# Kernel optimization log

Measured on AMD Instinct MI355X. Metric: run time of the kernel, lower is better.

The kernel has to match this reference:

```python
import jax, jax.numpy as jnp
import numpy as np

# weight_dict {0:1,1:1,2:1,3:1} with similarity_pyramid=True -> w_l = 1/2^l
WEIGHTS = [1.0, 0.5, 0.25, 0.125]
WINS = [9, 9, 7, 5]
NCC_FACTOR = 100.0
N_LOSSES = 2  # ['mse', 'ncc']


def _sliding_sum(x, win, axis):
    """Box (ones-kernel) sliding-window sum along one axis, 'same' output via
    zero padding of win//2 on each side -- separable equivalent of the dense
    ones-kernel conv in the original NCC_loss."""
    pad = win // 2
    pw = [(0, 0)] * x.ndim
    pw[axis] = (pad + 1, pad)  # extra leading zero so cumsum diff gives window sums
    c = jnp.cumsum(jnp.pad(x, pw), axis=axis)
    n = x.shape[axis]
    hi = jax.lax.slice_in_dim(c, win, win + n, axis=axis)
    lo = jax.lax.slice_in_dim(c, 0, n, axis=axis)
    return hi - lo


def _box_sum(x, win):
    # x: [B,1,H,W]; 2D box filter == separable 1D sliding sums
    return _sliding_sum(_sliding_sum(x, win, 2), win, 3)


def _ncc_loss(y_pred, y_true, win):
    Ii, Ji = y_true, y_pred
    ws = float(win * win)
    I_sum = _box_sum(Ii, win)
    J_sum = _box_sum(Ji, win)
    I2_sum = _box_sum(Ii * Ii, win)
    J2_sum = _box_sum(Ji * Ji, win)
    IJ_sum = _box_sum(Ii * Ji, win)
    u_I = I_sum / ws
    u_J = J_sum / ws
    cross = IJ_sum - u_J * I_sum - u_I * J_sum + u_I * u_J * ws
    I_var = I2_sum - 2.0 * u_I * I_sum + u_I * u_I * ws
    J_var = J2_sum - 2.0 * u_J * J_sum + u_J * u_J * ws
    cc = cross * cross / (I_var * J_var + 1e-8)
    return -jnp.sum(jnp.mean(cc, axis=0)) / NCC_FACTOR


def _l2_loss(inp, tgt):
    # sum over spatial dims, mean over batch & channel
    return jnp.mean(jnp.sum((inp - tgt) ** 2, axis=(2, 3)))


def _hier_loss(y_hats, y):
    total = jnp.zeros((), dtype=y.dtype)
    levels = []
    for l, yh in enumerate(y_hats):
        if yh.shape == y.shape:
            yt = y
        else:
            # F.interpolate bilinear align_corners=False == half-pixel linear resize
            yt = jax.image.resize(y, yh.shape, method='linear', antialias=False)
        w = WEIGHTS[l]
        ll = (w * _l2_loss(yh, yt) + w * _ncc_loss(yh, yt, WINS[l])) / N_LOSSES
        levels.append(ll)
        total = total + ll
    return total, levels


def setup_inputs() -> dict:
    key = jax.random.key(0)
    ks = jax.random.split(key, 5)
    return {
        'y_hat_0': jax.random.uniform(ks[0], (32, 1, 512, 512), dtype=jnp.float32),
        'y_hat_1': jax.random.uniform(ks[1], (32, 1, 256, 256), dtype=jnp.float32),
        'y_hat_2': jax.random.uniform(ks[2], (32, 1, 128, 128), dtype=jnp.float32),
        'y_hat_3': jax.random.uniform(ks[3], (32, 1, 64, 64), dtype=jnp.float32),
        'y': jax.random.uniform(ks[4], (32, 1, 512, 512), dtype=jnp.float32),
    }


def reference(y_hat_0, y_hat_1, y_hat_2, y_hat_3, y):
    total, levels = _hier_loss([y_hat_0, y_hat_1, y_hat_2, y_hat_3], y)
    return (total, *levels)
```

## Files before the change

kernel.cpp:

```cpp
#include <hip/hip_runtime.h>

#define NT 256
#define RCHUNK 32
#define NSLOT 32
#define RWMAX (NT + 8)

__device__ __forceinline__ float ccval(float sI, float sJ, float sII, float sJJ,
                                       float sIJ, float inv_ws) {
    float cross = fmaf(-(sI * sJ), inv_ws, sIJ);
    float iv    = fmaf(-(sI * sI), inv_ws, sII);
    float jv    = fmaf(-(sJ * sJ), inv_ws, sJJ);
    float den   = fmaf(iv, jv, 1e-8f);
    return (cross * cross) * __builtin_amdgcn_rcpf(den);
}

struct St { float J, i0, i1, i2, i3; };

template<int W, int H, int WIN, int S, int CW>
__device__ __forceinline__ void level_block(const float* __restrict__ yh,
                                            const float* __restrict__ y,
                                            int sub, float* __restrict__ ws_acc,
                                            int level,
                                            float (*bufI)[RWMAX], float (*bufJ)[RWMAX])
{
    constexpr int HW  = WIN / 2;
    constexpr int RW  = CW + 2 * HW;
    constexpr int T   = RCHUNK + 2 * HW;
    constexpr int G   = (T + WIN - 1) / WIN;
    constexpr int NIT = G * WIN;
    constexpr int OFF = (S - 2) / 2;
    constexpr int WRAP = RW - NT;
    constexpr float INV_WS = 1.0f / (float)(WIN * WIN);

    constexpr int STRIPS = W / CW;
    constexpr int CHUNKS = H / RCHUNK;

    int b     = sub / (STRIPS * CHUNKS);
    int rem   = sub - b * (STRIPS * CHUNKS);
    int chunk = rem / STRIPS;
    int strip = rem - chunk * STRIPS;
    int r0 = chunk * RCHUNK;
    int c0 = strip * CW;

    const float* Jb = yh + (size_t)b * (W * H);
    const float* Yb = y  + (size_t)b * (512 * 512);

    int t  = threadIdx.x;
    int jA = c0 - HW + t;
    int jB = jA + NT;

    auto fetch = [&](int rr, int j, St& s) {
        s.J = 0.f; s.i0 = 0.f; s.i1 = 0.f; s.i2 = 0.f; s.i3 = 0.f;
        int r = r0 - HW + rr;
        if (rr < NIT && r >= 0 && r < H && j >= 0 && j < W) {
            s.J = Jb[(size_t)r * W + j];
            if constexpr (S == 1) {
                s.i0 = Yb[(size_t)r * 512 + j];
            } else {
                int yr = S * r + OFF;
                const float* p = Yb + (size_t)yr * 512 + (S * j + OFF);
                s.i0 = p[0]; s.i1 = p[1]; s.i2 = p[512]; s.i3 = p[513];
            }
        }
    };
    auto ival = [&](const St& s) -> float {
        if constexpr (S == 1) return s.i0;
        else return 0.25f * ((s.i0 + s.i1) + (s.i2 + s.i3));
    };

    float rI[WIN], rJ[WIN], rII[WIN], rJJ[WIN], rIJ[WIN];
#pragma unroll
    for (int k = 0; k < WIN; ++k) { rI[k]=0.f; rJ[k]=0.f; rII[k]=0.f; rJJ[k]=0.f; rIJ[k]=0.f; }
    float vI=0.f, vJ=0.f, vII=0.f, vJJ=0.f, vIJ=0.f;
    float l2acc = 0.f, ccacc = 0.f;

    St sA, sB;
    fetch(0, jA, sA);
    sB.J = 0.f; sB.i0 = 0.f; sB.i1 = 0.f; sB.i2 = 0.f; sB.i3 = 0.f;
    if constexpr (WRAP > 0) { if (t < WRAP) fetch(0, jB, sB); }

    for (int g = 0; g < G; ++g) {
#pragma unroll
        for (int u = 0; u < WIN; ++u) {
            int rr = g * WIN + u;
            float* bI = bufI[rr & 1];
            float* bJ = bufJ[rr & 1];

            bI[t] = ival(sA);
            bJ[t] = sA.J;
            if constexpr (WRAP > 0) {
                if (t < WRAP) { bI[t + NT] = ival(sB); bJ[t + NT] = sB.J; }
            }
            fetch(rr + 1, jA, sA);
            if constexpr (WRAP > 0) { if (t < WRAP) fetch(rr + 1, jB, sB); }
            __syncthreads();
            if (t < CW) {
                float sIs=0.f, sJs=0.f, sIIs=0.f, sJJs=0.f, sIJs=0.f, Ic=0.f, Jc=0.f;
#pragma unroll
                for (int k = 0; k < WIN; ++k) {
                    float I = bI[t + k];
                    float J = bJ[t + k];
                    if (k == HW) { Ic = I; Jc = J; }
                    sIs += I; sJs += J;
                    sIIs = fmaf(I, I, sIIs);
                    sJJs = fmaf(J, J, sJJs);
                    sIJs = fmaf(I, J, sIJs);
                }
                if (rr >= HW && rr < HW + RCHUNK) {
                    float d = Jc - Ic;
                    l2acc = fmaf(d, d, l2acc);
                }
                rI[u]=sIs; rJ[u]=sJs; rII[u]=sIIs; rJJ[u]=sJJs; rIJ[u]=sIJs;
                vI+=sIs; vJ+=sJs; vII+=sIIs; vJJ+=sJJs; vIJ+=sIJs;
                if (rr >= 2 * HW && rr < T) {
                    ccacc += ccval(vI, vJ, vII, vJJ, vIJ, INV_WS);
                    const int uo = (u + 1) % WIN;
                    vI-=rI[uo]; vJ-=rJ[uo]; vII-=rII[uo]; vJJ-=rJJ[uo]; vIJ-=rIJ[uo];
                }
            }
        }
    }

#pragma unroll
    for (int off = 32; off > 0; off >>= 1) {
        l2acc += __shfl_down(l2acc, off);
        ccacc += __shfl_down(ccacc, off);
    }
    int lane = t & 63;
    if (lane == 0) {
        int slot = (blockIdx.x * 4 + (t >> 6)) & (NSLOT - 1);
        atomicAdd(&ws_acc[(level * 2 + 0) * NSLOT + slot], l2acc);
        atomicAdd(&ws_acc[(level * 2 + 1) * NSLOT + slot], ccacc);
    }
}

__global__ __launch_bounds__(NT)
void hier_loss_kernel(const float* __restrict__ yh0, const float* __restrict__ yh1,
                      const float* __restrict__ yh2, const float* __restrict__ yh3,
                      const float* __restrict__ y, float* ws_acc)
{
    __shared__ float bufI[2][RWMAX];
    __shared__ float bufJ[2][RWMAX];
    int bid = blockIdx.x;
    if (bid < 1024) {
        level_block<512, 512, 9, 1, 256>(yh0, y, bid, ws_acc, 0, bufI, bufJ);
    } else if (bid < 1280) {
        level_block<256, 256, 9, 2, 256>(yh1, y, bid - 1024, ws_acc, 1, bufI, bufJ);
    } else if (bid < 1408) {
        level_block<128, 128, 7, 4, 128>(yh2, y, bid - 1280, ws_acc, 2, bufI, bufJ);
    } else {
        level_block<64, 64, 5, 8, 64>(yh3, y, bid - 1408, ws_acc, 3, bufI, bufJ);
    }
}

__global__ void hier_finalize_kernel(const float* __restrict__ ws_acc, float* __restrict__ out)
{
    if (threadIdx.x == 0 && blockIdx.x == 0) {
        const float wts[4] = {1.0f, 0.5f, 0.25f, 0.125f};
        float total = 0.f;
#pragma unroll
        for (int lv = 0; lv < 4; ++lv) {
            float l2s = 0.f, ccs = 0.f;
            for (int s = 0; s < NSLOT; ++s) {
                l2s += ws_acc[(lv * 2 + 0) * NSLOT + s];
                ccs += ws_acc[(lv * 2 + 1) * NSLOT + s];
            }
            float l2  = l2s / 32.0f;
            float ncc = -ccs / (32.0f * 100.0f);
            float ll  = wts[lv] * (l2 + ncc) * 0.5f;
            out[1 + lv] = ll;
            total += ll;
        }
        out[0] = total;
    }
}

extern "C" void kernel_launch(void* const* d_in, const int* in_sizes, int n_in,
                              void* d_out, int out_size, void* d_ws, size_t ws_size,
                              hipStream_t stream)
{
    const float* yh0 = (const float*)d_in[0];
    const float* yh1 = (const float*)d_in[1];
    const float* yh2 = (const float*)d_in[2];
    const float* yh3 = (const float*)d_in[3];
    const float* y   = (const float*)d_in[4];
    float* ws_acc = (float*)d_ws;
    float* out = (float*)d_out;

    hipMemsetAsync(ws_acc, 0, 8 * NSLOT * sizeof(float), stream);
    hier_loss_kernel<<<1472, NT, 0, stream>>>(yh0, yh1, yh2, yh3, y, ws_acc);
    hier_finalize_kernel<<<1, 64, 0, stream>>>(ws_acc, out);
}
```

Before: 106.2 us.

## Stage full rows into LDS with direct global-to-LDS loads and multi-row phases

```diff
diff --git a/kernel.cpp b/kernel.cpp
--- a/kernel.cpp
+++ b/kernel.cpp
@@ -3,7 +3,21 @@
 #define NT 256
 #define RCHUNK 32
 #define NSLOT 32
-#define RWMAX (NT + 8)
+#define AC 4
+
+typedef float f2 __attribute__((ext_vector_type(2)));
+typedef float f4v __attribute__((ext_vector_type(4)));
+
+__device__ __forceinline__ void gll16(const float* g, float* l) {
+    __builtin_amdgcn_global_load_lds(
+        (const __attribute__((address_space(1))) void*)g,
+        (__attribute__((address_space(3))) void*)l, 16, 0, 0);
+}
+__device__ __forceinline__ void gll4(const float* g, float* l) {
+    __builtin_amdgcn_global_load_lds(
+        (const __attribute__((address_space(1))) void*)g,
+        (__attribute__((address_space(3))) void*)l, 4, 0, 0);
+}
 
 __device__ __forceinline__ float ccval(float sI, float sJ, float sII, float sJJ,
                                        float sIJ, float inv_ws) {
@@ -14,110 +28,194 @@
     return (cross * cross) * __builtin_amdgcn_rcpf(den);
 }
 
-struct St { float J, i0, i1, i2, i3; };
-
-template<int W, int H, int WIN, int S, int CW>
-__device__ __forceinline__ void level_block(const float* __restrict__ yh,
-                                            const float* __restrict__ y,
-                                            int sub, float* __restrict__ ws_acc,
-                                            int level,
-                                            float (*bufI)[RWMAX], float (*bufJ)[RWMAX])
-{
-    constexpr int HW  = WIN / 2;
-    constexpr int RW  = CW + 2 * HW;
-    constexpr int T   = RCHUNK + 2 * HW;
-    constexpr int G   = (T + WIN - 1) / WIN;
-    constexpr int NIT = G * WIN;
-    constexpr int OFF = (S - 2) / 2;
-    constexpr int WRAP = RW - NT;
+template<int W, int WIN, int S, int P>
+__device__ __forceinline__ void stage_phase(
+    float* __restrict__ smem, int parity, int k, int t,
+    const float* __restrict__ Jb, const float* __restrict__ Yb, int r0)
+{
+    constexpr int HW = WIN / 2;
+    constexpr int T = RCHUNK + 2 * HW;
+    constexpr int ROWSZ = W + 16;
+    constexpr bool B16 = (W >= 256);
+    constexpr int SEGW = B16 ? 256 : 64;
+    constexpr int SEGS = W / SEGW;
+    constexpr int NARR = (S == 1) ? 2 : 1;
+    int wv = t >> 6, ln = t & 63;
+    int fl = 0;
+#pragma unroll
+    for (int p = 0; p < P; ++p) {
+        int rr = k * P + p;
+        int r = r0 - HW + rr;
+        bool valid = (rr < T) && (r >= 0) && (r < W);
+        float* base = smem + (size_t)((parity * P + p) * 2) * ROWSZ;
+#pragma unroll
+        for (int a = 0; a < NARR; ++a) {
+            const float* srow;
+            float* drow;
+            if (a == NARR - 1) { srow = Jb + (long)r * W;   drow = base + ROWSZ; }
+            else               { srow = Yb + (long)r * 512; drow = base; }
+#pragma unroll
+            for (int sg = 0; sg < SEGS; ++sg) {
+                if ((fl & 3) == wv) {
+                    if (valid) {
+                        if constexpr (B16) gll16(srow + sg * 256 + 4 * ln, drow + AC + sg * 256);
+                        else               gll4 (srow + sg * 64 + ln,      drow + AC + sg * 64);
+                    } else {
+                        if constexpr (B16) {
+                            f4v z = {0.f, 0.f, 0.f, 0.f};
+                            *(f4v*)(drow + AC + sg * 256 + 4 * ln) = z;
+                        } else {
+                            drow[AC + sg * 64 + ln] = 0.f;
+                        }
+                    }
+                }
+                ++fl;
+            }
+        }
+        if constexpr (S >= 2) {
+            if (t < W) {
+                float v = 0.f;
+                if (valid) {
+                    if constexpr (S == 2) {
+                        const float* pp = Yb + (long)(2 * r) * 512 + 2 * t;
+                        f2 a2 = *(const f2*)pp;
+                        f2 b2 = *(const f2*)(pp + 512);
+                        v = 0.25f * ((a2.x + a2.y) + (b2.x + b2.y));
+                    } else {
+                        constexpr int OFF = (S - 2) / 2;
+                        const float* pp = Yb + (long)(S * r + OFF) * 512 + (S * t + OFF);
+                        v = 0.25f * ((pp[0] + pp[1]) + (pp[512] + pp[513]));
+                    }
+                }
+                base[AC + t] = v;
+            }
+        }
+    }
+}
+
+template<int W, int WIN, int P, int BASE, int CPT>
+__device__ __forceinline__ void compute_rows(
+    const float* __restrict__ smem, int parity, int k, int t,
+    float (&rI)[CPT][WIN], float (&rJ)[CPT][WIN], float (&rII)[CPT][WIN],
+    float (&rJJ)[CPT][WIN], float (&rIJ)[CPT][WIN],
+    float (&vI)[CPT], float (&vJ)[CPT], float (&vII)[CPT],
+    float (&vJJ)[CPT], float (&vIJ)[CPT],
+    float& l2acc, float& ccacc)
+{
+    constexpr int HW = WIN / 2;
+    constexpr int T = RCHUNK + 2 * HW;
+    constexpr int ROWSZ = W + 16;
+    constexpr int NB = (WIN + 2) / 2;
     constexpr float INV_WS = 1.0f / (float)(WIN * WIN);
-
-    constexpr int STRIPS = W / CW;
-    constexpr int CHUNKS = H / RCHUNK;
-
-    int b     = sub / (STRIPS * CHUNKS);
-    int rem   = sub - b * (STRIPS * CHUNKS);
-    int chunk = rem / STRIPS;
-    int strip = rem - chunk * STRIPS;
+#pragma unroll
+    for (int u = 0; u < P; ++u) {
+        int rr = k * P + u;
+        const float* bI = smem + (size_t)((parity * P + u) * 2) * ROWSZ;
+        const float* bJ = bI + ROWSZ;
+        if (rr < T) {
+#pragma unroll
+            for (int c = 0; c < CPT; ++c) {
+                int col = t + c * NT;
+                if (CPT * NT <= W || col < W) {
+                    int START = col - HW + AC;
+                    int e0 = START & ~1;
+                    bool sh = (START & 1) != 0;
+                    float LI[2 * NB], LJ[2 * NB];
+#pragma unroll
+                    for (int kk = 0; kk < NB; ++kk) {
+                        f2 a2 = *(const f2*)(bI + e0 + 2 * kk);
+                        f2 b2 = *(const f2*)(bJ + e0 + 2 * kk);
+                        LI[2 * kk] = a2.x; LI[2 * kk + 1] = a2.y;
+                        LJ[2 * kk] = b2.x; LJ[2 * kk + 1] = b2.y;
+                    }
+                    float sIs = 0.f, sJs = 0.f, sIIs = 0.f, sJJs = 0.f, sIJs = 0.f;
+#pragma unroll
+                    for (int kk = 0; kk < WIN; ++kk) {
+                        float I = sh ? LI[kk + 1] : LI[kk];
+                        float J = sh ? LJ[kk + 1] : LJ[kk];
+                        sIs += I; sJs += J;
+                        sIIs = fmaf(I, I, sIIs);
+                        sJJs = fmaf(J, J, sJJs);
+                        sIJs = fmaf(I, J, sIJs);
+                    }
+                    if (rr >= HW && rr < HW + RCHUNK) {
+                        float Ic = sh ? LI[HW + 1] : LI[HW];
+                        float Jc = sh ? LJ[HW + 1] : LJ[HW];
+                        float d = Jc - Ic;
+                        l2acc = fmaf(d, d, l2acc);
+                    }
+                    const int SL = (BASE + u) % WIN;
+                    rI[c][SL] = sIs; rJ[c][SL] = sJs; rII[c][SL] = sIIs;
+                    rJJ[c][SL] = sJJs; rIJ[c][SL] = sIJs;
+                    vI[c] += sIs; vJ[c] += sJs; vII[c] += sIIs;
+                    vJJ[c] += sJJs; vIJ[c] += sIJs;
+                    if (rr >= 2 * HW) {
+                        ccacc += ccval(vI[c], vJ[c], vII[c], vJJ[c], vIJ[c], INV_WS);
+                        const int SO = (BASE + u + 1) % WIN;
+                        vI[c] -= rI[c][SO]; vJ[c] -= rJ[c][SO]; vII[c] -= rII[c][SO];
+                        vJJ[c] -= rJJ[c][SO]; vIJ[c] -= rIJ[c][SO];
+                    }
+                }
+            }
+        }
+    }
+}
+
+template<int W, int WIN, int S, int P, int CPT>
+__device__ void level_block(const float* __restrict__ yh, const float* __restrict__ y,
+                            int sub, float* __restrict__ ws_acc, int level, float* smem)
+{
+    constexpr int HW = WIN / 2;
+    constexpr int T = RCHUNK + 2 * HW;
+    constexpr int NPH = (T + P - 1) / P;
+    constexpr int RES = WIN / P;
+    constexpr int NMACRO = (NPH + RES - 1) / RES;
+    constexpr int ROWSZ = W + 16;
+    constexpr int SMN = 2 * P * 2 * ROWSZ;
+
+    int b = sub & 31;
+    int chunk = sub >> 5;
     int r0 = chunk * RCHUNK;
-    int c0 = strip * CW;
-
-    const float* Jb = yh + (size_t)b * (W * H);
-    const float* Yb = y  + (size_t)b * (512 * 512);
-
-    int t  = threadIdx.x;
-    int jA = c0 - HW + t;
-    int jB = jA + NT;
-
-    auto fetch = [&](int rr, int j, St& s) {
-        s.J = 0.f; s.i0 = 0.f; s.i1 = 0.f; s.i2 = 0.f; s.i3 = 0.f;
-        int r = r0 - HW + rr;
-        if (rr < NIT && r >= 0 && r < H && j >= 0 && j < W) {
-            s.J = Jb[(size_t)r * W + j];
-            if constexpr (S == 1) {
-                s.i0 = Yb[(size_t)r * 512 + j];
-            } else {
-                int yr = S * r + OFF;
-                const float* p = Yb + (size_t)yr * 512 + (S * j + OFF);
-                s.i0 = p[0]; s.i1 = p[1]; s.i2 = p[512]; s.i3 = p[513];
-            }
-        }
-    };
-    auto ival = [&](const St& s) -> float {
-        if constexpr (S == 1) return s.i0;
-        else return 0.25f * ((s.i0 + s.i1) + (s.i2 + s.i3));
-    };
-
-    float rI[WIN], rJ[WIN], rII[WIN], rJJ[WIN], rIJ[WIN];
-#pragma unroll
-    for (int k = 0; k < WIN; ++k) { rI[k]=0.f; rJ[k]=0.f; rII[k]=0.f; rJJ[k]=0.f; rIJ[k]=0.f; }
-    float vI=0.f, vJ=0.f, vII=0.f, vJJ=0.f, vIJ=0.f;
+    const float* Jb = yh + (size_t)b * W * W;
+    const float* Yb = y + (size_t)b * 512 * 512;
+    int t = threadIdx.x;
+
+    for (int i = t; i < SMN; i += NT) smem[i] = 0.f;
+    __syncthreads();
+
+    float rI[CPT][WIN], rJ[CPT][WIN], rII[CPT][WIN], rJJ[CPT][WIN], rIJ[CPT][WIN];
+    float vI[CPT], vJ[CPT], vII[CPT], vJJ[CPT], vIJ[CPT];
+#pragma unroll
+    for (int c = 0; c < CPT; ++c) {
+#pragma unroll
+        for (int kk = 0; kk < WIN; ++kk) {
+            rI[c][kk] = 0.f; rJ[c][kk] = 0.f; rII[c][kk] = 0.f;
+            rJJ[c][kk] = 0.f; rIJ[c][kk] = 0.f;
+        }
+        vI[c] = 0.f; vJ[c] = 0.f; vII[c] = 0.f; vJJ[c] = 0.f; vIJ[c] = 0.f;
+    }
     float l2acc = 0.f, ccacc = 0.f;
 
-    St sA, sB;
-    fetch(0, jA, sA);
-    sB.J = 0.f; sB.i0 = 0.f; sB.i1 = 0.f; sB.i2 = 0.f; sB.i3 = 0.f;
-    if constexpr (WRAP > 0) { if (t < WRAP) fetch(0, jB, sB); }
-
-    for (int g = 0; g < G; ++g) {
-#pragma unroll
-        for (int u = 0; u < WIN; ++u) {
-            int rr = g * WIN + u;
-            float* bI = bufI[rr & 1];
-            float* bJ = bufJ[rr & 1];
-
-            bI[t] = ival(sA);
-            bJ[t] = sA.J;
-            if constexpr (WRAP > 0) {
-                if (t < WRAP) { bI[t + NT] = ival(sB); bJ[t + NT] = sB.J; }
-            }
-            fetch(rr + 1, jA, sA);
-            if constexpr (WRAP > 0) { if (t < WRAP) fetch(rr + 1, jB, sB); }
-            __syncthreads();
-            if (t < CW) {
-                float sIs=0.f, sJs=0.f, sIIs=0.f, sJJs=0.f, sIJs=0.f, Ic=0.f, Jc=0.f;
-#pragma unroll
-                for (int k = 0; k < WIN; ++k) {
-                    float I = bI[t + k];
-                    float J = bJ[t + k];
-                    if (k == HW) { Ic = I; Jc = J; }
-                    sIs += I; sJs += J;
-                    sIIs = fmaf(I, I, sIIs);
-                    sJJs = fmaf(J, J, sJJs);
-                    sIJs = fmaf(I, J, sIJs);
-                }
-                if (rr >= HW && rr < HW + RCHUNK) {
-                    float d = Jc - Ic;
-                    l2acc = fmaf(d, d, l2acc);
-                }
-                rI[u]=sIs; rJ[u]=sJs; rII[u]=sIIs; rJJ[u]=sJJs; rIJ[u]=sIJs;
-                vI+=sIs; vJ+=sJs; vII+=sIIs; vJJ+=sJJs; vIJ+=sIJs;
-                if (rr >= 2 * HW && rr < T) {
-                    ccacc += ccval(vI, vJ, vII, vJJ, vIJ, INV_WS);
-                    const int uo = (u + 1) % WIN;
-                    vI-=rI[uo]; vJ-=rJ[uo]; vII-=rII[uo]; vJJ-=rJJ[uo]; vIJ-=rIJ[uo];
-                }
-            }
+    stage_phase<W, WIN, S, P>(smem, 0, 0, t, Jb, Yb, r0);
+
+    for (int m = 0; m < NMACRO; ++m) {
+#pragma unroll
+        for (int j = 0; j < RES; ++j) {
+            int k = m * RES + j;
+            asm volatile("s_waitcnt vmcnt(0) lgkmcnt(0)" ::: "memory");
+            __builtin_amdgcn_s_barrier();
+            asm volatile("" ::: "memory");
+            if (k + 1 < NPH)
+                stage_phase<W, WIN, S, P>(smem, (k + 1) & 1, k + 1, t, Jb, Yb, r0);
+            if (j == 0)
+                compute_rows<W, WIN, P, 0, CPT>(smem, k & 1, k, t, rI, rJ, rII, rJJ, rIJ,
+                                                vI, vJ, vII, vJJ, vIJ, l2acc, ccacc);
+            else if (j == 1)
+                compute_rows<W, WIN, P, (P) % WIN, CPT>(smem, k & 1, k, t, rI, rJ, rII, rJJ, rIJ,
+                                                        vI, vJ, vII, vJJ, vIJ, l2acc, ccacc);
+            else
+                compute_rows<W, WIN, P, (2 * P) % WIN, CPT>(smem, k & 1, k, t, rI, rJ, rII, rJJ, rIJ,
+                                                            vI, vJ, vII, vJJ, vIJ, l2acc, ccacc);
         }
     }
 
@@ -126,8 +224,7 @@
         l2acc += __shfl_down(l2acc, off);
         ccacc += __shfl_down(ccacc, off);
     }
-    int lane = t & 63;
-    if (lane == 0) {
+    if ((t & 63) == 0) {
         int slot = (blockIdx.x * 4 + (t >> 6)) & (NSLOT - 1);
         atomicAdd(&ws_acc[(level * 2 + 0) * NSLOT + slot], l2acc);
         atomicAdd(&ws_acc[(level * 2 + 1) * NSLOT + slot], ccacc);
@@ -139,17 +236,16 @@
                       const float* __restrict__ yh2, const float* __restrict__ yh3,
                       const float* __restrict__ y, float* ws_acc)
 {
-    __shared__ float bufI[2][RWMAX];
-    __shared__ float bufJ[2][RWMAX];
+    __shared__ float smem[6336];
     int bid = blockIdx.x;
-    if (bid < 1024) {
-        level_block<512, 512, 9, 1, 256>(yh0, y, bid, ws_acc, 0, bufI, bufJ);
-    } else if (bid < 1280) {
-        level_block<256, 256, 9, 2, 256>(yh1, y, bid - 1024, ws_acc, 1, bufI, bufJ);
-    } else if (bid < 1408) {
-        level_block<128, 128, 7, 4, 128>(yh2, y, bid - 1280, ws_acc, 2, bufI, bufJ);
+    if (bid < 512) {
+        level_block<512, 9, 1, 3, 2>(yh0, y, bid, ws_acc, 0, smem);
+    } else if (bid < 768) {
+        level_block<256, 9, 2, 3, 1>(yh1, y, bid - 512, ws_acc, 1, smem);
+    } else if (bid < 896) {
+        level_block<128, 7, 4, 7, 1>(yh2, y, bid - 768, ws_acc, 2, smem);
     } else {
-        level_block<64, 64, 5, 8, 64>(yh3, y, bid - 1408, ws_acc, 3, bufI, bufJ);
+        level_block<64, 5, 8, 5, 1>(yh3, y, bid - 896, ws_acc, 3, smem);
     }
 }
 
@@ -188,6 +284,6 @@
     float* out = (float*)d_out;
 
     hipMemsetAsync(ws_acc, 0, 8 * NSLOT * sizeof(float), stream);
-    hier_loss_kernel<<<1472, NT, 0, stream>>>(yh0, yh1, yh2, yh3, y, ws_acc);
+    hier_loss_kernel<<<960, NT, 0, stream>>>(yh0, yh1, yh2, yh3, y, ws_acc);
     hier_finalize_kernel<<<1, 64, 0, stream>>>(ws_acc, out);
 }
```

Result: slower. 283.7 us (+167.1%).

## Make each wavefront own a 64-column strip and drop block barriers

Applied to the files above, without the earlier changes.

```diff
diff --git a/kernel.cpp b/kernel.cpp
--- a/kernel.cpp
+++ b/kernel.cpp
@@ -3,7 +3,9 @@
 #define NT 256
 #define RCHUNK 32
 #define NSLOT 32
-#define RWMAX (NT + 8)
+#define RWA 72
+
+typedef float f2 __attribute__((ext_vector_type(2)));
 
 __device__ __forceinline__ float ccval(float sI, float sJ, float sII, float sJJ,
                                        float sIJ, float inv_ws) {
@@ -16,49 +18,47 @@
 
 struct St { float J, i0, i1, i2, i3; };
 
-template<int W, int H, int WIN, int S, int CW>
-__device__ __forceinline__ void level_block(const float* __restrict__ yh,
-                                            const float* __restrict__ y,
-                                            int sub, float* __restrict__ ws_acc,
-                                            int level,
-                                            float (*bufI)[RWMAX], float (*bufJ)[RWMAX])
-{
-    constexpr int HW  = WIN / 2;
-    constexpr int RW  = CW + 2 * HW;
-    constexpr int T   = RCHUNK + 2 * HW;
-    constexpr int G   = (T + WIN - 1) / WIN;
+template<int W, int WIN, int S>
+__device__ void level_wave(const float* __restrict__ yh,
+                           const float* __restrict__ y,
+                           int sub, float* __restrict__ ws_acc, int level,
+                           float* __restrict__ slab, int wid)
+{
+    constexpr int HW = WIN / 2;
+    constexpr int RW = 64 + 2 * HW;
+    constexpr int T  = RCHUNK + 2 * HW;
+    constexpr int G  = (T + WIN - 1) / WIN;
     constexpr int NIT = G * WIN;
+    constexpr int WRAP = RW - 64;
+    constexpr int NB = (WIN + 2) / 2;
     constexpr int OFF = (S - 2) / 2;
-    constexpr int WRAP = RW - NT;
     constexpr float INV_WS = 1.0f / (float)(WIN * WIN);
-
-    constexpr int STRIPS = W / CW;
-    constexpr int CHUNKS = H / RCHUNK;
+    constexpr int STRIPS = W / 64;
+    constexpr int CHUNKS = W / RCHUNK;
 
     int b     = sub / (STRIPS * CHUNKS);
     int rem   = sub - b * (STRIPS * CHUNKS);
     int chunk = rem / STRIPS;
     int strip = rem - chunk * STRIPS;
     int r0 = chunk * RCHUNK;
-    int c0 = strip * CW;
-
-    const float* Jb = yh + (size_t)b * (W * H);
-    const float* Yb = y  + (size_t)b * (512 * 512);
-
-    int t  = threadIdx.x;
-    int jA = c0 - HW + t;
-    int jB = jA + NT;
-
-    auto fetch = [&](int rr, int j, St& s) {
+    int c0 = strip * 64;
+
+    const float* Jb = yh + (size_t)b * W * W;
+    const float* Yb = y  + (size_t)b * 512 * 512;
+
+    int l  = threadIdx.x & 63;
+    int jA = c0 - HW + l;
+    int jB = jA + 64;
+
+    auto fetch1 = [&](int rr, int j, St& s) {
         s.J = 0.f; s.i0 = 0.f; s.i1 = 0.f; s.i2 = 0.f; s.i3 = 0.f;
         int r = r0 - HW + rr;
-        if (rr < NIT && r >= 0 && r < H && j >= 0 && j < W) {
-            s.J = Jb[(size_t)r * W + j];
+        if (rr < NIT && r >= 0 && r < W && j >= 0 && j < W) {
+            s.J = Jb[(long)r * W + j];
             if constexpr (S == 1) {
-                s.i0 = Yb[(size_t)r * 512 + j];
+                s.i0 = Yb[(long)r * 512 + j];
             } else {
-                int yr = S * r + OFF;
-                const float* p = Yb + (size_t)yr * 512 + (S * j + OFF);
+                const float* p = Yb + (long)(S * r + OFF) * 512 + (S * j + OFF);
                 s.i0 = p[0]; s.i1 = p[1]; s.i2 = p[512]; s.i3 = p[513];
             }
         }
@@ -75,44 +75,53 @@
     float l2acc = 0.f, ccacc = 0.f;
 
     St sA, sB;
-    fetch(0, jA, sA);
+    fetch1(0, jA, sA);
     sB.J = 0.f; sB.i0 = 0.f; sB.i1 = 0.f; sB.i2 = 0.f; sB.i3 = 0.f;
-    if constexpr (WRAP > 0) { if (t < WRAP) fetch(0, jB, sB); }
+    if (l < WRAP) fetch1(0, jB, sB);
 
     for (int g = 0; g < G; ++g) {
 #pragma unroll
         for (int u = 0; u < WIN; ++u) {
             int rr = g * WIN + u;
-            float* bI = bufI[rr & 1];
-            float* bJ = bufJ[rr & 1];
-
-            bI[t] = ival(sA);
-            bJ[t] = sA.J;
-            if constexpr (WRAP > 0) {
-                if (t < WRAP) { bI[t + NT] = ival(sB); bJ[t + NT] = sB.J; }
-            }
-            fetch(rr + 1, jA, sA);
-            if constexpr (WRAP > 0) { if (t < WRAP) fetch(rr + 1, jB, sB); }
-            __syncthreads();
-            if (t < CW) {
-                float sIs=0.f, sJs=0.f, sIIs=0.f, sJJs=0.f, sIJs=0.f, Ic=0.f, Jc=0.f;
-#pragma unroll
-                for (int k = 0; k < WIN; ++k) {
-                    float I = bI[t + k];
-                    float J = bJ[t + k];
-                    if (k == HW) { Ic = I; Jc = J; }
+            float* bI = slab + (size_t)(((rr & 1) * 2 + 0) * RWA);
+            float* bJ = slab + (size_t)(((rr & 1) * 2 + 1) * RWA);
+
+            bI[l] = ival(sA);
+            bJ[l] = sA.J;
+            if (l < WRAP) { bI[64 + l] = ival(sB); bJ[64 + l] = sB.J; }
+            fetch1(rr + 1, jA, sA);
+            if (l < WRAP) fetch1(rr + 1, jB, sB);
+            asm volatile("s_waitcnt lgkmcnt(0)" ::: "memory");
+            if (rr < T) {
+                int e0 = l & ~1;
+                bool sh = (l & 1) != 0;
+                float LI[2 * NB], LJ[2 * NB];
+#pragma unroll
+                for (int kk = 0; kk < NB; ++kk) {
+                    f2 a2 = *(const f2*)(bI + e0 + 2 * kk);
+                    f2 b2 = *(const f2*)(bJ + e0 + 2 * kk);
+                    LI[2 * kk] = a2.x; LI[2 * kk + 1] = a2.y;
+                    LJ[2 * kk] = b2.x; LJ[2 * kk + 1] = b2.y;
+                }
+                float sIs=0.f, sJs=0.f, sIIs=0.f, sJJs=0.f, sIJs=0.f;
+#pragma unroll
+                for (int kk = 0; kk < WIN; ++kk) {
+                    float I = sh ? LI[kk + 1] : LI[kk];
+                    float J = sh ? LJ[kk + 1] : LJ[kk];
                     sIs += I; sJs += J;
                     sIIs = fmaf(I, I, sIIs);
                     sJJs = fmaf(J, J, sJJs);
                     sIJs = fmaf(I, J, sIJs);
                 }
                 if (rr >= HW && rr < HW + RCHUNK) {
+                    float Ic = sh ? LI[HW + 1] : LI[HW];
+                    float Jc = sh ? LJ[HW + 1] : LJ[HW];
                     float d = Jc - Ic;
                     l2acc = fmaf(d, d, l2acc);
                 }
                 rI[u]=sIs; rJ[u]=sJs; rII[u]=sIIs; rJJ[u]=sJJs; rIJ[u]=sIJs;
                 vI+=sIs; vJ+=sJs; vII+=sIIs; vJJ+=sJJs; vIJ+=sIJs;
-                if (rr >= 2 * HW && rr < T) {
+                if (rr >= 2 * HW) {
                     ccacc += ccval(vI, vJ, vII, vJJ, vIJ, INV_WS);
                     const int uo = (u + 1) % WIN;
                     vI-=rI[uo]; vJ-=rJ[uo]; vII-=rII[uo]; vJJ-=rJJ[uo]; vIJ-=rIJ[uo];
@@ -126,9 +135,8 @@
         l2acc += __shfl_down(l2acc, off);
         ccacc += __shfl_down(ccacc, off);
     }
-    int lane = t & 63;
-    if (lane == 0) {
-        int slot = (blockIdx.x * 4 + (t >> 6)) & (NSLOT - 1);
+    if (l == 0) {
+        int slot = wid & (NSLOT - 1);
         atomicAdd(&ws_acc[(level * 2 + 0) * NSLOT + slot], l2acc);
         atomicAdd(&ws_acc[(level * 2 + 1) * NSLOT + slot], ccacc);
     }
@@ -139,17 +147,19 @@
                       const float* __restrict__ yh2, const float* __restrict__ yh3,
                       const float* __restrict__ y, float* ws_acc)
 {
-    __shared__ float bufI[2][RWMAX];
-    __shared__ float bufJ[2][RWMAX];
-    int bid = blockIdx.x;
-    if (bid < 1024) {
-        level_block<512, 512, 9, 1, 256>(yh0, y, bid, ws_acc, 0, bufI, bufJ);
-    } else if (bid < 1280) {
-        level_block<256, 256, 9, 2, 256>(yh1, y, bid - 1024, ws_acc, 1, bufI, bufJ);
-    } else if (bid < 1408) {
-        level_block<128, 128, 7, 4, 128>(yh2, y, bid - 1280, ws_acc, 2, bufI, bufJ);
+    __shared__ float smem[4][2][2][RWA];
+    int wave = threadIdx.x >> 6;
+    float* slab = &smem[wave][0][0][0];
+
+    int wid = blockIdx.x * (NT / 64) + wave;
+    if (wid < 4096) {
+        level_wave<512, 9, 1>(yh0, y, wid, ws_acc, 0, slab, wid);
+    } else if (wid < 5120) {
+        level_wave<256, 9, 2>(yh1, y, wid - 4096, ws_acc, 1, slab, wid);
+    } else if (wid < 5376) {
+        level_wave<128, 7, 4>(yh2, y, wid - 5120, ws_acc, 2, slab, wid);
     } else {
-        level_block<64, 64, 5, 8, 64>(yh3, y, bid - 1408, ws_acc, 3, bufI, bufJ);
+        level_wave<64, 5, 8>(yh3, y, wid - 5376, ws_acc, 3, slab, wid);
     }
 }
 
@@ -188,6 +198,6 @@
     float* out = (float*)d_out;
 
     hipMemsetAsync(ws_acc, 0, 8 * NSLOT * sizeof(float), stream);
-    hier_loss_kernel<<<1472, NT, 0, stream>>>(yh0, yh1, yh2, yh3, y, ws_acc);
+    hier_loss_kernel<<<5440 / (NT / 64), NT, 0, stream>>>(yh0, yh1, yh2, yh3, y, ws_acc);
     hier_finalize_kernel<<<1, 64, 0, stream>>>(ws_acc, out);
 }
```

Result: slower. 215.7 us (+103.1%).

## Batch row fetches into WIN-row phases with double-buffered interleaved LDS

Applied to the files above, without the earlier changes.

```diff
diff --git a/kernel.cpp b/kernel.cpp
--- a/kernel.cpp
+++ b/kernel.cpp
@@ -3,7 +3,9 @@
 #define NT 256
 #define RCHUNK 32
 #define NSLOT 32
-#define RWMAX (NT + 8)
+#define RWA 272
+
+typedef float f2 __attribute__((ext_vector_type(2)));
 
 __device__ __forceinline__ float ccval(float sI, float sJ, float sII, float sJJ,
                                        float sIJ, float inv_ws) {
@@ -14,26 +16,21 @@
     return (cross * cross) * __builtin_amdgcn_rcpf(den);
 }
 
-struct St { float J, i0, i1, i2, i3; };
-
-template<int W, int H, int WIN, int S, int CW>
-__device__ __forceinline__ void level_block(const float* __restrict__ yh,
-                                            const float* __restrict__ y,
-                                            int sub, float* __restrict__ ws_acc,
-                                            int level,
-                                            float (*bufI)[RWMAX], float (*bufJ)[RWMAX])
+template<int W, int WIN, int S, int CW>
+__device__ void level_block(const float* __restrict__ yh,
+                            const float* __restrict__ y,
+                            int sub, float* __restrict__ ws_acc, int level,
+                            float* __restrict__ sm)
 {
     constexpr int HW  = WIN / 2;
     constexpr int RW  = CW + 2 * HW;
     constexpr int T   = RCHUNK + 2 * HW;
-    constexpr int G   = (T + WIN - 1) / WIN;
-    constexpr int NIT = G * WIN;
+    constexpr int NPH = (T + WIN - 1) / WIN;
     constexpr int OFF = (S - 2) / 2;
-    constexpr int WRAP = RW - NT;
+    constexpr int WRAP = (RW > NT) ? (RW - NT) : 0;
     constexpr float INV_WS = 1.0f / (float)(WIN * WIN);
-
     constexpr int STRIPS = W / CW;
-    constexpr int CHUNKS = H / RCHUNK;
+    constexpr int CHUNKS = W / RCHUNK;
 
     int b     = sub / (STRIPS * CHUNKS);
     int rem   = sub - b * (STRIPS * CHUNKS);
@@ -42,30 +39,53 @@
     int r0 = chunk * RCHUNK;
     int c0 = strip * CW;
 
-    const float* Jb = yh + (size_t)b * (W * H);
-    const float* Yb = y  + (size_t)b * (512 * 512);
-
-    int t  = threadIdx.x;
-    int jA = c0 - HW + t;
-    int jB = jA + NT;
-
-    auto fetch = [&](int rr, int j, St& s) {
-        s.J = 0.f; s.i0 = 0.f; s.i1 = 0.f; s.i2 = 0.f; s.i3 = 0.f;
+    const float* Jb = yh + (size_t)b * W * W;
+    const float* Yb = y  + (size_t)b * 512 * 512;
+    int t = threadIdx.x;
+    int colA = c0 - HW + t;
+    int colB = colA + NT;
+
+    float fI[WIN], fJ[WIN], gI[WIN], gJ[WIN];
+
+    auto fetch_one = [&](int rr, int col, float& I, float& J) {
+        I = 0.f; J = 0.f;
         int r = r0 - HW + rr;
-        if (rr < NIT && r >= 0 && r < H && j >= 0 && j < W) {
-            s.J = Jb[(size_t)r * W + j];
+        if (rr < T && r >= 0 && r < W && col >= 0 && col < W) {
+            J = Jb[(long)r * W + col];
             if constexpr (S == 1) {
-                s.i0 = Yb[(size_t)r * 512 + j];
+                I = Yb[(long)r * 512 + col];
+            } else if constexpr (S == 2) {
+                const float* p = Yb + (long)(2 * r) * 512 + 2 * col;
+                f2 a = *(const f2*)p;
+                f2 c = *(const f2*)(p + 512);
+                I = 0.25f * ((a.x + a.y) + (c.x + c.y));
             } else {
-                int yr = S * r + OFF;
-                const float* p = Yb + (size_t)yr * 512 + (S * j + OFF);
-                s.i0 = p[0]; s.i1 = p[1]; s.i2 = p[512]; s.i3 = p[513];
+                const float* p = Yb + (long)(S * r + OFF) * 512 + (S * col + OFF);
+                I = 0.25f * ((p[0] + p[1]) + (p[512] + p[513]));
             }
         }
     };
-    auto ival = [&](const St& s) -> float {
-        if constexpr (S == 1) return s.i0;
-        else return 0.25f * ((s.i0 + s.i1) + (s.i2 + s.i3));
+
+    auto fetch_phase = [&](int k) {
+#pragma unroll
+        for (int p = 0; p < WIN; ++p) {
+            int rr = k * WIN + p;
+            if (t < RW) fetch_one(rr, colA, fI[p], fJ[p]);
+            if constexpr (WRAP > 0) {
+                if (t < WRAP) fetch_one(rr, colB, gI[p], gJ[p]);
+            }
+        }
+    };
+
+    auto write_phase = [&](int k) {
+#pragma unroll
+        for (int p = 0; p < WIN; ++p) {
+            float* base = sm + 2 * (size_t)(((k & 1) * WIN + p) * RWA);
+            if (t < RW) { f2 v = {fI[p], fJ[p]}; *(f2*)(base + 2 * t) = v; }
+            if constexpr (WRAP > 0) {
+                if (t < WRAP) { f2 v = {gI[p], gJ[p]}; *(f2*)(base + 2 * (t + NT)) = v; }
+            }
+        }
     };
 
     float rI[WIN], rJ[WIN], rII[WIN], rJJ[WIN], rIJ[WIN];
@@ -74,45 +94,36 @@
     float vI=0.f, vJ=0.f, vII=0.f, vJJ=0.f, vIJ=0.f;
     float l2acc = 0.f, ccacc = 0.f;
 
-    St sA, sB;
-    fetch(0, jA, sA);
-    sB.J = 0.f; sB.i0 = 0.f; sB.i1 = 0.f; sB.i2 = 0.f; sB.i3 = 0.f;
-    if constexpr (WRAP > 0) { if (t < WRAP) fetch(0, jB, sB); }
-
-    for (int g = 0; g < G; ++g) {
+    fetch_phase(0);
+
+    for (int k = 0; k < NPH; ++k) {
+        write_phase(k);
+        if (k + 1 < NPH) fetch_phase(k + 1);
+        asm volatile("s_waitcnt lgkmcnt(0)" ::: "memory");
+        __builtin_amdgcn_s_barrier();
 #pragma unroll
         for (int u = 0; u < WIN; ++u) {
-            int rr = g * WIN + u;
-            float* bI = bufI[rr & 1];
-            float* bJ = bufJ[rr & 1];
-
-            bI[t] = ival(sA);
-            bJ[t] = sA.J;
-            if constexpr (WRAP > 0) {
-                if (t < WRAP) { bI[t + NT] = ival(sB); bJ[t + NT] = sB.J; }
-            }
-            fetch(rr + 1, jA, sA);
-            if constexpr (WRAP > 0) { if (t < WRAP) fetch(rr + 1, jB, sB); }
-            __syncthreads();
-            if (t < CW) {
-                float sIs=0.f, sJs=0.f, sIIs=0.f, sJJs=0.f, sIJs=0.f, Ic=0.f, Jc=0.f;
-#pragma unroll
-                for (int k = 0; k < WIN; ++k) {
-                    float I = bI[t + k];
-                    float J = bJ[t + k];
-                    if (k == HW) { Ic = I; Jc = J; }
-                    sIs += I; sJs += J;
-                    sIIs = fmaf(I, I, sIIs);
-                    sJJs = fmaf(J, J, sJJs);
-                    sIJs = fmaf(I, J, sIJs);
+            int rr = k * WIN + u;
+            if (t < CW && rr < T) {
+                const float* base = sm + 2 * (size_t)(((k & 1) * WIN + u) * RWA);
+                float sI=0.f, sJ=0.f, sII=0.f, sJJ=0.f, sIJ=0.f, Ic=0.f, Jc=0.f;
+#pragma unroll
+                for (int kk = 0; kk < WIN; ++kk) {
+                    f2 v = *(const f2*)(base + 2 * (t + kk));
+                    float I = v.x, J = v.y;
+                    if (kk == HW) { Ic = I; Jc = J; }
+                    sI += I; sJ += J;
+                    sII = fmaf(I, I, sII);
+                    sJJ = fmaf(J, J, sJJ);
+                    sIJ = fmaf(I, J, sIJ);
                 }
                 if (rr >= HW && rr < HW + RCHUNK) {
                     float d = Jc - Ic;
                     l2acc = fmaf(d, d, l2acc);
                 }
-                rI[u]=sIs; rJ[u]=sJs; rII[u]=sIIs; rJJ[u]=sJJs; rIJ[u]=sIJs;
-                vI+=sIs; vJ+=sJs; vII+=sIIs; vJJ+=sJJs; vIJ+=sIJs;
-                if (rr >= 2 * HW && rr < T) {
+                rI[u]=sI; rJ[u]=sJ; rII[u]=sII; rJJ[u]=sJJ; rIJ[u]=sIJ;
+                vI+=sI; vJ+=sJ; vII+=sII; vJJ+=sJJ; vIJ+=sIJ;
+                if (rr >= 2 * HW) {
                     ccacc += ccval(vI, vJ, vII, vJJ, vIJ, INV_WS);
                     const int uo = (u + 1) % WIN;
                     vI-=rI[uo]; vJ-=rJ[uo]; vII-=rII[uo]; vJJ-=rJJ[uo]; vIJ-=rIJ[uo];
@@ -126,8 +137,7 @@
         l2acc += __shfl_down(l2acc, off);
         ccacc += __shfl_down(ccacc, off);
     }
-    int lane = t & 63;
-    if (lane == 0) {
+    if ((t & 63) == 0) {
         int slot = (blockIdx.x * 4 + (t >> 6)) & (NSLOT - 1);
         atomicAdd(&ws_acc[(level * 2 + 0) * NSLOT + slot], l2acc);
         atomicAdd(&ws_acc[(level * 2 + 1) * NSLOT + slot], ccacc);
@@ -139,17 +149,16 @@
                       const float* __restrict__ yh2, const float* __restrict__ yh3,
                       const float* __restrict__ y, float* ws_acc)
 {
-    __shared__ float bufI[2][RWMAX];
-    __shared__ float bufJ[2][RWMAX];
+    __shared__ float smem[2 * 9 * RWA * 2];
     int bid = blockIdx.x;
     if (bid < 1024) {
-        level_block<512, 512, 9, 1, 256>(yh0, y, bid, ws_acc, 0, bufI, bufJ);
+        level_block<512, 9, 1, 256>(yh0, y, bid, ws_acc, 0, smem);
     } else if (bid < 1280) {
-        level_block<256, 256, 9, 2, 256>(yh1, y, bid - 1024, ws_acc, 1, bufI, bufJ);
+        level_block<256, 9, 2, 256>(yh1, y, bid - 1024, ws_acc, 1, smem);
     } else if (bid < 1408) {
-        level_block<128, 128, 7, 4, 128>(yh2, y, bid - 1280, ws_acc, 2, bufI, bufJ);
+        level_block<128, 7, 4, 128>(yh2, y, bid - 1280, ws_acc, 2, smem);
     } else {
-        level_block<64, 64, 5, 8, 64>(yh3, y, bid - 1408, ws_acc, 3, bufI, bufJ);
+        level_block<64, 5, 8, 64>(yh3, y, bid - 1408, ws_acc, 3, smem);
     }
 }
 
```

Result: slower. 117.6 us (+10.7%).
